# Optimization experiments

Hardware: AMD Instinct MI355X
Metric: run time of the kernel (lower is better)

Reference implementation:

```python
import jax, jax.numpy as jnp
import numpy as np

VOCAB, D_EMB, Z_DIM, HID = 32000, 512, 256, 1024
B, T = 32, 128
PAD_IDX = 0

def setup_inputs() -> dict:
    key = jax.random.key(0)
    ks = jax.random.split(key, 12)
    s_emb = 1.0  # nn.Embedding default N(0,1)
    u = lambda k, shape, fan: jax.random.uniform(k, shape, jnp.float32, -1.0, 1.0) / np.sqrt(fan)
    emb = jax.random.normal(ks[0], (VOCAB, D_EMB), jnp.float32) * s_emb
    emb = emb.at[PAD_IDX].set(0.0)  # padding_idx row zeroed
    inp = {
        "z": jax.random.normal(ks[1], (B, Z_DIM), jnp.float32),
        "x": jax.random.randint(ks[2], (B, T), 0, VOCAB, jnp.int32),
        "W_h": u(ks[3], (HID, Z_DIM), Z_DIM),
        "b_h": u(ks[4], (HID,), Z_DIM),
        "emb": emb,
        "W_ih": u(ks[5], (4 * HID, D_EMB), HID),
        "W_hh": u(ks[6], (4 * HID, HID), HID),
        "b_ih": u(ks[7], (4 * HID,), HID),
        "b_hh": u(ks[8], (4 * HID,), HID),
        "W_out": u(ks[9], (VOCAB, HID), HID),
        "b_out": u(ks[10], (VOCAB,), HID),
    }
    return inp

def _lstm_decode(z, x, W_h, b_h, emb, W_ih, W_hh, b_ih, b_hh, W_out, b_out):
    h0 = jnp.tanh(z @ W_h.T + b_h)            # [B, H]
    c0 = jnp.zeros_like(h0)
    e = emb[x]                                 # [B, T, D]
    # Precompute input-side gate projections for all timesteps at once.
    x_gates = jnp.einsum('btd,gd->btg', e, W_ih) + b_ih + b_hh  # [B, T, 4H]
    x_gates_t = jnp.swapaxes(x_gates, 0, 1)    # [T, B, 4H]

    def step(carry, xg_t):
        h, c = carry
        gates = xg_t + h @ W_hh.T              # [B, 4H]
        i, f, g, o = jnp.split(gates, 4, axis=-1)  # torch gate order i,f,g,o
        i, f, o = jax.nn.sigmoid(i), jax.nn.sigmoid(f), jax.nn.sigmoid(o)
        g = jnp.tanh(g)
        c = f * c + i * g
        h = o * jnp.tanh(c)
        return (h, c), h

    _, hs = jax.lax.scan(step, (h0, c0), x_gates_t)  # hs: [T, B, H]
    out = jnp.swapaxes(hs, 0, 1)               # [B, T, H]
    return jnp.einsum('bth,vh->btv', out, W_out) + b_out  # [B, T, V]

def reference(z, x, W_h, b_h, emb, W_ih, W_hh, b_ih, b_hh, W_out, b_out):
    return _lstm_decode(z, x, W_h, b_h, emb, W_ih, W_hh, b_ih, b_hh, W_out, b_out)
```

## Files before the change

### kernel.cpp

```cpp
#include <hip/hip_runtime.h>

typedef _Float16 f16;
typedef _Float16 f16x8 __attribute__((ext_vector_type(8)));
typedef _Float16 f16x4 __attribute__((ext_vector_type(4)));
typedef float    f32x4 __attribute__((ext_vector_type(4)));
typedef unsigned long long ull;

static constexpr int Bb  = 32;
static constexpr int Tt  = 128;
static constexpr int HID = 1024;
static constexpr int ZD  = 256;
static constexpr int DE  = 512;
static constexpr int VOC = 32000;
static constexpr int BT  = Bb * Tt;
static constexpr int G4  = 4 * HID;
static constexpr int NLSTM = 64;
static constexpr int NCOL  = 125;

__device__ __forceinline__ void gld_lds16(const void* g, void* l) {
  __builtin_amdgcn_global_load_lds((const __attribute__((address_space(1))) unsigned int*)g,
                                   (__attribute__((address_space(3))) unsigned int*)l,
                                   16, 0, 0);
}

__global__ void cvt_kernel(const float* __restrict__ s, f16* __restrict__ d, int n4) {
  int i = blockIdx.x * blockDim.x + threadIdx.x;
  int st = gridDim.x * blockDim.x;
  for (; i < n4; i += st) {
    float4 v = ((const float4*)s)[i];
    f16x4 o = { (f16)v.x, (f16)v.y, (f16)v.z, (f16)v.w };
    ((f16x4*)d)[i] = o;
  }
}

__global__ void gather_kernel(const float* __restrict__ emb, const int* __restrict__ x,
                              f16* __restrict__ E) {
  int g = blockIdx.x * 256 + threadIdx.x;
  int m = g >> 6, seg = (g & 63) * 8;
  int idx = x[m];
  const float* src = emb + (size_t)idx * DE + seg;
  float4 a = *(const float4*)src;
  float4 b = *(const float4*)(src + 4);
  f16x8 o = { (f16)a.x,(f16)a.y,(f16)a.z,(f16)a.w,(f16)b.x,(f16)b.y,(f16)b.z,(f16)b.w };
  *(f16x8*)(E + (size_t)m * DE + seg) = o;
}

__global__ void bsum_kernel(const float* __restrict__ a, const float* __restrict__ b,
                            float* __restrict__ o, int n) {
  int i = blockIdx.x * blockDim.x + threadIdx.x;
  if (i < n) o[i] = a[i] + b[i];
}

__global__ __launch_bounds__(256) void h0_kernel(const float* __restrict__ z,
                                                 const float* __restrict__ W_h,
                                                 const float* __restrict__ b_h,
                                                 f16* __restrict__ h0f) {
  __shared__ float zs[32][260];
  __shared__ float wsl[8][260];
  const int jc = blockIdx.x, tid = threadIdx.x;
  #pragma unroll
  for (int it = 0; it < 8; ++it) {
    int idx = it * 256 + tid;
    float4 v = ((const float4*)z)[idx];
    int b = idx >> 6, k = (idx & 63) * 4;
    zs[b][k] = v.x; zs[b][k+1] = v.y; zs[b][k+2] = v.z; zs[b][k+3] = v.w;
  }
  #pragma unroll
  for (int it = 0; it < 2; ++it) {
    int idx = it * 256 + tid;
    float4 v = ((const float4*)(W_h + (size_t)jc * 8 * ZD))[idx];
    int r = idx >> 6, k = (idx & 63) * 4;
    wsl[r][k] = v.x; wsl[r][k+1] = v.y; wsl[r][k+2] = v.z; wsl[r][k+3] = v.w;
  }
  __syncthreads();
  const int b = tid >> 3, jj = tid & 7;
  const int j = jc * 8 + jj;
  float acc = b_h[j];
  for (int k = 0; k < ZD; ++k) acc += zs[b][k] * wsl[jj][k];
  h0f[(size_t)b * HID + j] = (f16)tanhf(acc);
}

__global__ __launch_bounds__(256, 2) void gemmxg_kernel(
    const f16* __restrict__ A, const f16* __restrict__ B,
    const float* __restrict__ bias, float* __restrict__ C,
    int M, int N, int K) {
  __shared__ f16 As[128 * 64];
  __shared__ f16 Bs[128 * 64];
  const int n0 = blockIdx.x * 128, m0 = blockIdx.y * 128;
  const int tid = threadIdx.x, wid = tid >> 6, lane = tid & 63;
  const int wm = wid >> 1, wn = wid & 1;
  const int sr = lane >> 3, sk = (lane & 7) * 8;
  f32x4 acc[4][4] = {};
  for (int k0 = 0; k0 < K; k0 += 64) {
    __syncthreads();
    #pragma unroll
    for (int i = 0; i < 4; ++i) {
      int rr = (wid * 4 + i) * 8;
      gld_lds16(A + (size_t)(m0 + rr + sr) * K + k0 + sk, &As[rr * 64]);
      gld_lds16(B + (size_t)(n0 + rr + sr) * K + k0 + sk, &Bs[rr * 64]);
    }
    __syncthreads();
    #pragma unroll
    for (int ks = 0; ks < 2; ++ks) {
      f16x8 af[4], bf[4];
      #pragma unroll
      for (int mt = 0; mt < 4; ++mt)
        af[mt] = *(const f16x8*)&As[(wm * 64 + mt * 16 + (lane & 15)) * 64 + ks * 32 + (lane >> 4) * 8];
      #pragma unroll
      for (int nt = 0; nt < 4; ++nt)
        bf[nt] = *(const f16x8*)&Bs[(wn * 64 + nt * 16 + (lane & 15)) * 64 + ks * 32 + (lane >> 4) * 8];
      #pragma unroll
      for (int mt = 0; mt < 4; ++mt)
        #pragma unroll
        for (int nt = 0; nt < 4; ++nt)
          acc[mt][nt] = __builtin_amdgcn_mfma_f32_16x16x32_f16(af[mt], bf[nt], acc[mt][nt], 0, 0, 0);
    }
  }
  #pragma unroll
  for (int nt = 0; nt < 4; ++nt) {
    int col = n0 + wn * 64 + nt * 16 + (lane & 15);
    float bv = bias[col];
    #pragma unroll
    for (int mt = 0; mt < 4; ++mt) {
      int row = m0 + wm * 64 + mt * 16 + (lane >> 4) * 4;
      int b = row >> 7, t0 = row & 127;
      float4 v = { acc[mt][nt][0] + bv, acc[mt][nt][1] + bv,
                   acc[mt][nt][2] + bv, acc[mt][nt][3] + bv };
      *(float4*)&C[((size_t)col * 32 + b) * 128 + t0] = v;
    }
  }
}

static constexpr int SM_HL   = 0;
static constexpr int SM_PART = 66048;
static constexpr int SM_FL   = 133632;
static constexpr int SM_SIZE = 133904;

__device__ void lstm_role(const f16* __restrict__ Whh16, const float* __restrict__ XG2,
                          const f16* __restrict__ h0f, f16* __restrict__ HS,
                          unsigned* __restrict__ bar, unsigned* __restrict__ gready,
                          char* smem) {
  const int bid = blockIdx.x, tid = threadIdx.x;
  const int lane = tid & 63, wid = tid >> 6;
  const int lr = lane & 15, hi = lane >> 4;
  const int j0 = bid * 16;
  f16 (*hl)[1032] = (f16 (*)[1032])(smem + SM_HL);
  float (*part)[64][33] = (float (*)[64][33])(smem + SM_PART);
  unsigned* fl = (unsigned*)(smem + SM_FL);

  if (tid < 64) fl[tid] = 0;

  f16x8 wfrag[4][4];
  #pragma unroll
  for (int rt = 0; rt < 4; ++rt) {
    int g = rt * HID + j0 + lr;
    #pragma unroll
    for (int kk = 0; kk < 4; ++kk)
      wfrag[rt][kk] = *(const f16x8*)(Whh16 + (size_t)g * HID + wid * 128 + kk * 32 + hi * 8);
  }

  const int ub = tid & 15, bb = tid >> 4;
  float creg = 0.f;
  __syncthreads();

  for (int t = 0; t < Tt; ++t) {
    float xg[4];
    #pragma unroll
    for (int q = 0; q < 4; ++q)
      xg[q] = XG2[((size_t)(q * HID + j0 + ub) * 32 + bb) * 128 + t];

    if (t > 0) {
      if (wid == 0) {
        for (;;) {
          unsigned f = __hip_atomic_load(&bar[lane], __ATOMIC_RELAXED, __HIP_MEMORY_SCOPE_AGENT);
          __hip_atomic_store(&fl[lane], f, __ATOMIC_RELAXED, __HIP_MEMORY_SCOPE_WORKGROUP);
          if (__all(f >= (unsigned)t)) break;
        }
        if (bid == 0 && lane == 0)
          __hip_atomic_store(gready, (unsigned)t, __ATOMIC_RELAXED, __HIP_MEMORY_SCOPE_AGENT);
      } else {
        const int p = wid * 8 + (lane & 7);
        for (;;) {
          unsigned f = __hip_atomic_load(&fl[p], __ATOMIC_RELAXED, __HIP_MEMORY_SCOPE_WORKGROUP);
          if (__all(f >= (unsigned)t)) break;
        }
      }
    }

    {
      const int uo = wid * 128 + (lane & 31) * 4;
      #pragma unroll
      for (int ps = 0; ps < 16; ++ps) {
        int row = ps * 2 + (lane >> 5);
        const f16* hb = (t == 0) ? (h0f + (size_t)row * HID)
                                 : (HS + (size_t)((t - 1) * 32 + row) * HID);
        ull v = *(const ull*)(hb + uo);
        *(ull*)&hl[row][uo] = v;
      }
    }

    {
      f32x4 acc[4][2] = {};
      #pragma unroll
      for (int kk = 0; kk < 4; ++kk) {
        int ko = wid * 128 + kk * 32 + hi * 8;
        f16x8 bf0 = *(const f16x8*)&hl[lr][ko];
        f16x8 bf1 = *(const f16x8*)&hl[16 + lr][ko];
        #pragma unroll
        for (int rt = 0; rt < 4; ++rt) {
          acc[rt][0] = __builtin_amdgcn_mfma_f32_16x16x32_f16(wfrag[rt][kk], bf0, acc[rt][0], 0, 0, 0);
          acc[rt][1] = __builtin_amdgcn_mfma_f32_16x16x32_f16(wfrag[rt][kk], bf1, acc[rt][1], 0, 0, 0);
        }
      }
      #pragma unroll
      for (int rt = 0; rt < 4; ++rt)
        #pragma unroll
        for (int bt = 0; bt < 2; ++bt)
          #pragma unroll
          for (int p = 0; p < 4; ++p)
            part[wid][rt * 16 + hi * 4 + p][bt * 16 + lr] = acc[rt][bt][p];
    }
    __syncthreads();

    {
      float g4[4];
      #pragma unroll
      for (int q = 0; q < 4; ++q) {
        int i = q * 16 + ub;
        float s = xg[q];
        #pragma unroll
        for (int w = 0; w < 8; ++w) s += part[w][i][bb];
        g4[q] = s;
      }
      float ig = 1.f / (1.f + __expf(-g4[0]));
      float fg = 1.f / (1.f + __expf(-g4[1]));
      float gg = tanhf(g4[2]);
      float og = 1.f / (1.f + __expf(-g4[3]));
      creg = fg * creg + ig * gg;
      float h = og * tanhf(creg);
      union { f16 h; unsigned short u; } cv;
      cv.h = (f16)h;
      __hip_atomic_store((unsigned short*)&HS[(size_t)(t * 32 + bb) * HID + j0 + ub],
                         cv.u, __ATOMIC_RELAXED, __HIP_MEMORY_SCOPE_AGENT);
    }

    asm volatile("s_waitcnt vmcnt(0)" ::: "memory");
    __syncthreads();
    if (tid == 0)
      __hip_atomic_store(&bar[bid], (unsigned)(t + 1),
                         __ATOMIC_RELAXED, __HIP_MEMORY_SCOPE_AGENT);
  }

  if (bid == 0) {
    if (wid == 0) {
      for (;;) {
        unsigned f = __hip_atomic_load(&bar[lane], __ATOMIC_RELAXED, __HIP_MEMORY_SCOPE_AGENT);
        if (__all(f >= (unsigned)Tt)) break;
      }
      if (lane == 0)
        __hip_atomic_store(gready, (unsigned)Tt, __ATOMIC_RELAXED, __HIP_MEMORY_SCOPE_AGENT);
    }
    __syncthreads();
  }
}

__device__ void worker_role(const f16* __restrict__ HS, const f16* __restrict__ Wout16,
                            const float* __restrict__ b_out, float* __restrict__ out,
                            unsigned* __restrict__ gready, char* smem) {
  const int ng = blockIdx.x - NLSTM;
  const int tid = threadIdx.x, wid = tid >> 6, lane = tid & 63;
  const int wm = wid >> 2, wn = wid & 3;
  const int lr = lane & 15, hi = lane >> 4;
  const int srow = lane >> 2;
  const int scol = ((lane & 3) ^ ((lane >> 3) & 3)) * 8;
  const int sx   = (hi ^ ((lr >> 1) & 3)) * 8;
  f16* As = (f16*)(smem);
  f16* Bs = (f16*)(smem + 65536);
  const int cb0 = wid * 2, cb1 = wid * 2 + 1;
  const int n0 = ng * 256;

  for (int mg = 0; mg < 16; ++mg) {
    if (wid == 0) {
      const unsigned tgt = (unsigned)(8 * mg + 8);
      for (;;) {
        unsigned g = __hip_atomic_load(gready, __ATOMIC_RELAXED, __HIP_MEMORY_SCOPE_AGENT);
        if (g >= tgt) break;
        __builtin_amdgcn_s_sleep(64);
      }
    }
    __syncthreads();

    const int m0 = mg * 256;
    f32x4 acc[8][4] = {};

    auto STAGE = [&](int kt) {
      const int k0 = kt << 5, buf = kt & 3;
      gld_lds16(HS     + (size_t)(m0 + cb0 * 16 + srow) * HID + k0 + scol, As + buf * 8192 + cb0 * 512);
      gld_lds16(Wout16 + (size_t)(n0 + cb0 * 16 + srow) * HID + k0 + scol, Bs + buf * 8192 + cb0 * 512);
      gld_lds16(HS     + (size_t)(m0 + cb1 * 16 + srow) * HID + k0 + scol, As + buf * 8192 + cb1 * 512);
      gld_lds16(Wout16 + (size_t)(n0 + cb1 * 16 + srow) * HID + k0 + scol, Bs + buf * 8192 + cb1 * 512);
    };

    STAGE(0); STAGE(1); STAGE(2);
    for (int kt = 0; kt < 32; ++kt) {
      if (kt < 30)       asm volatile("s_waitcnt vmcnt(8)" ::: "memory");
      else if (kt == 30) asm volatile("s_waitcnt vmcnt(4)" ::: "memory");
      else               asm volatile("s_waitcnt vmcnt(0)" ::: "memory");
      __builtin_amdgcn_s_barrier();
      if (kt + 3 < 32) STAGE(kt + 3);
      const f16* as = As + (kt & 3) * 8192;
      const f16* bs = Bs + (kt & 3) * 8192;
      f16x8 af[8], bf[4];
      #pragma unroll
      for (int mt = 0; mt < 8; ++mt)
        af[mt] = *(const f16x8*)&as[(wm * 128 + mt * 16 + lr) * 32 + sx];
      #pragma unroll
      for (int nt = 0; nt < 4; ++nt)
        bf[nt] = *(const f16x8*)&bs[(wn * 64 + nt * 16 + lr) * 32 + sx];
      __builtin_amdgcn_s_setprio(1);
      #pragma unroll
      for (int mt = 0; mt < 8; ++mt)
        #pragma unroll
        for (int nt = 0; nt < 4; ++nt)
          acc[mt][nt] = __builtin_amdgcn_mfma_f32_16x16x32_f16(af[mt], bf[nt], acc[mt][nt], 0, 0, 0);
      __builtin_amdgcn_s_setprio(0);
    }

    #pragma unroll
    for (int nt = 0; nt < 4; ++nt) {
      int col = n0 + wn * 64 + nt * 16 + lr;
      float bv = b_out[col];
      #pragma unroll
      for (int mt = 0; mt < 8; ++mt) {
        int mbase = m0 + wm * 128 + mt * 16 + hi * 4;
        #pragma unroll
        for (int p = 0; p < 4; ++p) {
          int mp = mbase + p;
          int orow = (mp & 31) * 128 + (mp >> 5);
          __builtin_nontemporal_store(acc[mt][nt][p] + bv,
                                      &out[(size_t)orow * VOC + col]);
        }
      }
    }
    __syncthreads();
  }
}

__global__ __launch_bounds__(512, 1) void fused_kernel(
    const f16* __restrict__ Whh16, const float* __restrict__ XG2,
    const f16* __restrict__ h0f, f16* __restrict__ HS,
    const f16* __restrict__ Wout16, const float* __restrict__ b_out,
    float* __restrict__ out, unsigned* __restrict__ bar,
    unsigned* __restrict__ gready) {
  __shared__ __align__(16) char smem[SM_SIZE];
  if (blockIdx.x < NLSTM) {
    lstm_role(Whh16, XG2, h0f, HS, bar, gready, smem);
  } else if (blockIdx.x < NLSTM + NCOL) {
    worker_role(HS, Wout16, b_out, out, gready, smem);
  }
}

extern "C" void kernel_launch(void* const* d_in, const int* in_sizes, int n_in,
                              void* d_out, int out_size, void* d_ws, size_t ws_size,
                              hipStream_t stream) {
  const float* z     = (const float*)d_in[0];
  const int*   x     = (const int*)d_in[1];
  const float* W_h   = (const float*)d_in[2];
  const float* b_h   = (const float*)d_in[3];
  const float* emb   = (const float*)d_in[4];
  const float* W_ih  = (const float*)d_in[5];
  const float* W_hh  = (const float*)d_in[6];
  const float* b_ih  = (const float*)d_in[7];
  const float* b_hh  = (const float*)d_in[8];
  const float* W_out = (const float*)d_in[9];
  const float* b_out = (const float*)d_in[10];
  float* out = (float*)d_out;

  char* ws = (char*)d_ws;
  size_t off = 0;
  auto carve = [&](size_t n) { char* p = ws + off; off += (n + 255) & ~(size_t)255; return p; };
  f16*   E16    = (f16*)carve((size_t)BT * DE * 2);
  f16*   Wih16  = (f16*)carve((size_t)G4 * DE * 2);
  f16*   Whh16  = (f16*)carve((size_t)G4 * HID * 2);
  f16*   Wout16 = (f16*)carve((size_t)VOC * HID * 2);
  float* XG2    = (float*)carve((size_t)BT * G4 * 4);
  f16*   HS     = (f16*)carve((size_t)BT * HID * 2);
  f16*   h0f    = (f16*)carve((size_t)Bb * HID * 2);
  float* bs     = (float*)carve((size_t)G4 * 4);
  unsigned* bar    = (unsigned*)carve(256);
  unsigned* gready = (unsigned*)carve(256);

  (void)hipMemsetAsync(bar, 0, 512, stream);

  cvt_kernel<<<2048, 256, 0, stream>>>(W_ih,  Wih16,  G4 * DE / 4);
  cvt_kernel<<<2048, 256, 0, stream>>>(W_hh,  Whh16,  G4 * HID / 4);
  cvt_kernel<<<2048, 256, 0, stream>>>(W_out, Wout16, VOC * HID / 4);
  gather_kernel<<<BT * DE / 8 / 256, 256, 0, stream>>>(emb, x, E16);
  bsum_kernel<<<16, 256, 0, stream>>>(b_ih, b_hh, bs, G4);
  h0_kernel<<<128, 256, 0, stream>>>(z, W_h, b_h, h0f);

  dim3 g1(G4 / 128, BT / 128);
  gemmxg_kernel<<<g1, 256, 0, stream>>>(E16, Wih16, bs, XG2, BT, G4, DE);

  fused_kernel<<<256, 512, 0, stream>>>(Whh16, XG2, h0f, HS, Wout16, b_out, out,
                                        bar, gready);
}
```

Before: 806.0 us.

## Fold input-gate GEMM into fused kernel worker blocks and merge weight conversions

Removes the standalone gemmxg launch. The 125 worker blocks of the fused kernel now compute the x_gates tiles first, then signal through an atomic counter that the LSTM blocks wait on before their recurrence. The three weight conversion kernels are merged into one launch, and worker blocks add a staggered busy-wait delay before each output tile, presumably to spread out memory traffic. The aim is to cut launch overhead and kernel-boundary gaps. The cost is extra spin-wait synchronisation, and the GEMM runs on only half the threads of each 512-thread worker block.

```diff
diff --git a/kernel.cpp b/kernel.cpp
--- a/kernel.cpp
+++ b/kernel.cpp
@@ -16,6 +16,7 @@
 static constexpr int G4  = 4 * HID;
 static constexpr int NLSTM = 64;
 static constexpr int NCOL  = 125;
+static constexpr int NXGT  = 1024;
 
 __device__ __forceinline__ void gld_lds16(const void* g, void* l) {
   __builtin_amdgcn_global_load_lds((const __attribute__((address_space(1))) unsigned int*)g,
@@ -23,13 +24,20 @@
                                    16, 0, 0);
 }
 
-__global__ void cvt_kernel(const float* __restrict__ s, f16* __restrict__ d, int n4) {
+__global__ void cvt3_kernel(const float* __restrict__ a, f16* __restrict__ da, int na4,
+                            const float* __restrict__ b, f16* __restrict__ db, int nb4,
+                            const float* __restrict__ c, f16* __restrict__ dc, int nc4) {
   int i = blockIdx.x * blockDim.x + threadIdx.x;
   int st = gridDim.x * blockDim.x;
-  for (; i < n4; i += st) {
-    float4 v = ((const float4*)s)[i];
+  int tot = na4 + nb4 + nc4;
+  for (; i < tot; i += st) {
+    const float* s; f16* d; int j = i;
+    if (j < na4)              { s = a; d = da; }
+    else if ((j -= na4) < nb4){ s = b; d = db; }
+    else                      { j -= nb4; s = c; d = dc; }
+    float4 v = ((const float4*)s)[j];
     f16x4 o = { (f16)v.x, (f16)v.y, (f16)v.z, (f16)v.w };
-    ((f16x4*)d)[i] = o;
+    ((f16x4*)d)[j] = o;
   }
 }
 
@@ -80,57 +88,6 @@
   h0f[(size_t)b * HID + j] = (f16)tanhf(acc);
 }
 
-__global__ __launch_bounds__(256, 2) void gemmxg_kernel(
-    const f16* __restrict__ A, const f16* __restrict__ B,
-    const float* __restrict__ bias, float* __restrict__ C,
-    int M, int N, int K) {
-  __shared__ f16 As[128 * 64];
-  __shared__ f16 Bs[128 * 64];
-  const int n0 = blockIdx.x * 128, m0 = blockIdx.y * 128;
-  const int tid = threadIdx.x, wid = tid >> 6, lane = tid & 63;
-  const int wm = wid >> 1, wn = wid & 1;
-  const int sr = lane >> 3, sk = (lane & 7) * 8;
-  f32x4 acc[4][4] = {};
-  for (int k0 = 0; k0 < K; k0 += 64) {
-    __syncthreads();
-    #pragma unroll
-    for (int i = 0; i < 4; ++i) {
-      int rr = (wid * 4 + i) * 8;
-      gld_lds16(A + (size_t)(m0 + rr + sr) * K + k0 + sk, &As[rr * 64]);
-      gld_lds16(B + (size_t)(n0 + rr + sr) * K + k0 + sk, &Bs[rr * 64]);
-    }
-    __syncthreads();
-    #pragma unroll
-    for (int ks = 0; ks < 2; ++ks) {
-      f16x8 af[4], bf[4];
-      #pragma unroll
-      for (int mt = 0; mt < 4; ++mt)
-        af[mt] = *(const f16x8*)&As[(wm * 64 + mt * 16 + (lane & 15)) * 64 + ks * 32 + (lane >> 4) * 8];
-      #pragma unroll
-      for (int nt = 0; nt < 4; ++nt)
-        bf[nt] = *(const f16x8*)&Bs[(wn * 64 + nt * 16 + (lane & 15)) * 64 + ks * 32 + (lane >> 4) * 8];
-      #pragma unroll
-      for (int mt = 0; mt < 4; ++mt)
-        #pragma unroll
-        for (int nt = 0; nt < 4; ++nt)
-          acc[mt][nt] = __builtin_amdgcn_mfma_f32_16x16x32_f16(af[mt], bf[nt], acc[mt][nt], 0, 0, 0);
-    }
-  }
-  #pragma unroll
-  for (int nt = 0; nt < 4; ++nt) {
-    int col = n0 + wn * 64 + nt * 16 + (lane & 15);
-    float bv = bias[col];
-    #pragma unroll
-    for (int mt = 0; mt < 4; ++mt) {
-      int row = m0 + wm * 64 + mt * 16 + (lane >> 4) * 4;
-      int b = row >> 7, t0 = row & 127;
-      float4 v = { acc[mt][nt][0] + bv, acc[mt][nt][1] + bv,
-                   acc[mt][nt][2] + bv, acc[mt][nt][3] + bv };
-      *(float4*)&C[((size_t)col * 32 + b) * 128 + t0] = v;
-    }
-  }
-}
-
 static constexpr int SM_HL   = 0;
 static constexpr int SM_PART = 66048;
 static constexpr int SM_FL   = 133632;
@@ -139,7 +96,7 @@
 __device__ void lstm_role(const f16* __restrict__ Whh16, const float* __restrict__ XG2,
                           const f16* __restrict__ h0f, f16* __restrict__ HS,
                           unsigned* __restrict__ bar, unsigned* __restrict__ gready,
-                          char* smem) {
+                          unsigned* __restrict__ xgdone, char* smem) {
   const int bid = blockIdx.x, tid = threadIdx.x;
   const int lane = tid & 63, wid = tid >> 6;
   const int lr = lane & 15, hi = lane >> 4;
@@ -158,6 +115,13 @@
     for (int kk = 0; kk < 4; ++kk)
       wfrag[rt][kk] = *(const f16x8*)(Whh16 + (size_t)g * HID + wid * 128 + kk * 32 + hi * 8);
   }
+
+  if (tid == 0) {
+    while (__hip_atomic_load(xgdone, __ATOMIC_RELAXED, __HIP_MEMORY_SCOPE_AGENT) < (unsigned)NCOL)
+      __builtin_amdgcn_s_sleep(16);
+  }
+  __syncthreads();
+  __builtin_amdgcn_fence(__ATOMIC_ACQUIRE, "agent");
 
   const int ub = tid & 15, bb = tid >> 4;
   float creg = 0.f;
@@ -266,7 +230,10 @@
 
 __device__ void worker_role(const f16* __restrict__ HS, const f16* __restrict__ Wout16,
                             const float* __restrict__ b_out, float* __restrict__ out,
-                            unsigned* __restrict__ gready, char* smem) {
+                            unsigned* __restrict__ gready, unsigned* __restrict__ xgdone,
+                            const f16* __restrict__ E16, const f16* __restrict__ Wih16,
+                            const float* __restrict__ bs, float* __restrict__ XG2,
+                            char* smem) {
   const int ng = blockIdx.x - NLSTM;
   const int tid = threadIdx.x, wid = tid >> 6, lane = tid & 63;
   const int wm = wid >> 2, wn = wid & 3;
@@ -279,6 +246,69 @@
   const int cb0 = wid * 2, cb1 = wid * 2 + 1;
   const int n0 = ng * 256;
 
+  {
+    f16* As2 = (f16*)(smem);
+    f16* Bs2 = (f16*)(smem + 16384);
+    const bool act = tid < 256;
+    const int w4 = tid >> 6;
+    const int wmx = (w4 >> 1) & 1, wnx = w4 & 1;
+    const int sr = lane >> 3, sk = (lane & 7) * 8;
+    for (int xt = ng; xt < NXGT; xt += NCOL) {
+      const int xn = xt & 31, xm = xt >> 5;
+      const int n0x = xn * 128, m0x = xm * 128;
+      f32x4 xacc[4][4] = {};
+      for (int k0 = 0; k0 < DE; k0 += 64) {
+        __syncthreads();
+        if (act) {
+          #pragma unroll
+          for (int i = 0; i < 4; ++i) {
+            int rr = (w4 * 4 + i) * 8;
+            gld_lds16(E16   + (size_t)(m0x + rr + sr) * DE + k0 + sk, As2 + rr * 64);
+            gld_lds16(Wih16 + (size_t)(n0x + rr + sr) * DE + k0 + sk, Bs2 + rr * 64);
+          }
+        }
+        __syncthreads();
+        if (act) {
+          #pragma unroll
+          for (int ks = 0; ks < 2; ++ks) {
+            f16x8 af[4], bf[4];
+            #pragma unroll
+            for (int mt = 0; mt < 4; ++mt)
+              af[mt] = *(const f16x8*)&As2[(wmx * 64 + mt * 16 + lr) * 64 + ks * 32 + hi * 8];
+            #pragma unroll
+            for (int nt = 0; nt < 4; ++nt)
+              bf[nt] = *(const f16x8*)&Bs2[(wnx * 64 + nt * 16 + lr) * 64 + ks * 32 + hi * 8];
+            #pragma unroll
+            for (int mt = 0; mt < 4; ++mt)
+              #pragma unroll
+              for (int nt = 0; nt < 4; ++nt)
+                xacc[mt][nt] = __builtin_amdgcn_mfma_f32_16x16x32_f16(af[mt], bf[nt], xacc[mt][nt], 0, 0, 0);
+          }
+        }
+      }
+      if (act) {
+        #pragma unroll
+        for (int nt = 0; nt < 4; ++nt) {
+          int col = n0x + wnx * 64 + nt * 16 + lr;
+          float bv = bs[col];
+          #pragma unroll
+          for (int mt = 0; mt < 4; ++mt) {
+            int row = m0x + wmx * 64 + mt * 16 + hi * 4;
+            int b = row >> 7, t0 = row & 127;
+            float4 v = { xacc[mt][nt][0] + bv, xacc[mt][nt][1] + bv,
+                         xacc[mt][nt][2] + bv, xacc[mt][nt][3] + bv };
+            *(float4*)&XG2[((size_t)col * 32 + b) * 128 + t0] = v;
+          }
+        }
+      }
+      __syncthreads();
+    }
+    __threadfence();
+    __syncthreads();
+    if (tid == 0)
+      __hip_atomic_fetch_add(xgdone, 1u, __ATOMIC_RELEASE, __HIP_MEMORY_SCOPE_AGENT);
+  }
+
   for (int mg = 0; mg < 16; ++mg) {
     if (wid == 0) {
       const unsigned tgt = (unsigned)(8 * mg + 8);
@@ -289,6 +319,11 @@
       }
     }
     __syncthreads();
+    {
+      ull t0 = __builtin_amdgcn_s_memtime();
+      ull dl = (ull)((ng & 31) * 100);
+      while (__builtin_amdgcn_s_memtime() - t0 < dl) { }
+    }
 
     const int m0 = mg * 256;
     f32x4 acc[8][4] = {};
@@ -309,14 +344,14 @@
       __builtin_amdgcn_s_barrier();
       if (kt + 3 < 32) STAGE(kt + 3);
       const f16* as = As + (kt & 3) * 8192;
-      const f16* bs = Bs + (kt & 3) * 8192;
+      const f16* bs2 = Bs + (kt & 3) * 8192;
       f16x8 af[8], bf[4];
       #pragma unroll
       for (int mt = 0; mt < 8; ++mt)
         af[mt] = *(const f16x8*)&as[(wm * 128 + mt * 16 + lr) * 32 + sx];
       #pragma unroll
       for (int nt = 0; nt < 4; ++nt)
-        bf[nt] = *(const f16x8*)&bs[(wn * 64 + nt * 16 + lr) * 32 + sx];
+        bf[nt] = *(const f16x8*)&bs2[(wn * 64 + nt * 16 + lr) * 32 + sx];
       __builtin_amdgcn_s_setprio(1);
       #pragma unroll
       for (int mt = 0; mt < 8; ++mt)
@@ -347,16 +382,18 @@
 }
 
 __global__ __launch_bounds__(512, 1) void fused_kernel(
-    const f16* __restrict__ Whh16, const float* __restrict__ XG2,
+    const f16* __restrict__ Whh16, const float* __restrict__ XG2c,
     const f16* __restrict__ h0f, f16* __restrict__ HS,
     const f16* __restrict__ Wout16, const float* __restrict__ b_out,
     float* __restrict__ out, unsigned* __restrict__ bar,
-    unsigned* __restrict__ gready) {
+    unsigned* __restrict__ gready, unsigned* __restrict__ xgdone,
+    const f16* __restrict__ E16, const f16* __restrict__ Wih16,
+    const float* __restrict__ bs, float* __restrict__ XG2) {
   __shared__ __align__(16) char smem[SM_SIZE];
   if (blockIdx.x < NLSTM) {
-    lstm_role(Whh16, XG2, h0f, HS, bar, gready, smem);
+    lstm_role(Whh16, XG2c, h0f, HS, bar, gready, xgdone, smem);
   } else if (blockIdx.x < NLSTM + NCOL) {
-    worker_role(HS, Wout16, b_out, out, gready, smem);
+    worker_role(HS, Wout16, b_out, out, gready, xgdone, E16, Wih16, bs, XG2, smem);
   }
 }
 
@@ -389,19 +426,17 @@
   float* bs     = (float*)carve((size_t)G4 * 4);
   unsigned* bar    = (unsigned*)carve(256);
   unsigned* gready = (unsigned*)carve(256);
-
-  (void)hipMemsetAsync(bar, 0, 512, stream);
-
-  cvt_kernel<<<2048, 256, 0, stream>>>(W_ih,  Wih16,  G4 * DE / 4);
-  cvt_kernel<<<2048, 256, 0, stream>>>(W_hh,  Whh16,  G4 * HID / 4);
-  cvt_kernel<<<2048, 256, 0, stream>>>(W_out, Wout16, VOC * HID / 4);
+  unsigned* xgdone = (unsigned*)carve(256);
+
+  (void)hipMemsetAsync(bar, 0, 768, stream);
+
+  cvt3_kernel<<<2048, 256, 0, stream>>>(W_ih,  Wih16,  G4 * DE / 4,
+                                        W_hh,  Whh16,  G4 * HID / 4,
+                                        W_out, Wout16, VOC * HID / 4);
   gather_kernel<<<BT * DE / 8 / 256, 256, 0, stream>>>(emb, x, E16);
   bsum_kernel<<<16, 256, 0, stream>>>(b_ih, b_hh, bs, G4);
   h0_kernel<<<128, 256, 0, stream>>>(z, W_h, b_h, h0f);
 
-  dim3 g1(G4 / 128, BT / 128);
-  gemmxg_kernel<<<g1, 256, 0, stream>>>(E16, Wih16, bs, XG2, BT, G4, DE);
-
   fused_kernel<<<256, 512, 0, stream>>>(Whh16, XG2, h0f, HS, Wout16, b_out, out,
-                                        bar, gready);
-}
+                                        bar, gready, xgdone, E16, Wih16, bs, XG2);
+}
```

New measurement: 892.0 us. 1.11x slower.
